# Kernel tuning notes

Measured on AMD Instinct MI355X. Metric: run time of the kernel, lower is better.

The kernel has to match this reference:

```python
import jax, jax.numpy as jnp
import numpy as np

H = 2048        # hidden_size
NH = 32         # num_heads
HD = H // NH    # head_dim = 64
S = 512         # seq_len
UP = 2          # upsample_ratio
SU = S * UP     # upsampled seq len = 1024
INTER = 5632    # GatedMLP intermediate: int(2048*4*2/3) rounded up to mult of 256
EPS = 1e-6
DEPTH = 1


def rmsnorm(x, w):
    var = jnp.mean(jnp.square(x), axis=-1, keepdims=True)
    return x * jax.lax.rsqrt(var + EPS) * w


def setup_inputs() -> dict:
    key = jax.random.key(0)
    ks = jax.random.split(key, 12)
    sc = 0.02
    return {
        "hidden_states": jax.random.normal(ks[0], (2, S, H), dtype=jnp.float32),
        "W_up": jax.random.normal(ks[1], (SU, S), dtype=jnp.float32) * sc,
        "b_up": jnp.zeros((SU,), dtype=jnp.float32),
        "attn_norm_w": jnp.ones((H,), dtype=jnp.float32),
        "Wq": jax.random.normal(ks[2], (H, H), dtype=jnp.float32) * sc,
        "Wk": jax.random.normal(ks[3], (H, H), dtype=jnp.float32) * sc,
        "Wv": jax.random.normal(ks[4], (H, H), dtype=jnp.float32) * sc,
        "Wo": jax.random.normal(ks[5], (H, H), dtype=jnp.float32) * sc,
        "mlp_norm_w": jnp.ones((H,), dtype=jnp.float32),
        "Wg": jax.random.normal(ks[6], (INTER, H), dtype=jnp.float32) * sc,
        "Wu": jax.random.normal(ks[7], (INTER, H), dtype=jnp.float32) * sc,
        "Wd": jax.random.normal(ks[8], (H, INTER), dtype=jnp.float32) * sc,
    }


def reference(hidden_states, W_up, b_up, attn_norm_w, Wq, Wk, Wv, Wo,
              mlp_norm_w, Wg, Wu, Wd):
    B = hidden_states.shape[0]
    # init_upsampled_tokens: Linear over the sequence axis
    # up[b,t,d] = sum_s h[b,s,d] * W_up[t,s] + b_up[t]
    up = jnp.einsum('bsd,ts->btd', hidden_states, W_up) + b_up[None, :, None]

    for _ in range(DEPTH):
        residual = jnp.concatenate([hidden_states, up], axis=-2)  # [B, S+SU, H]
        x = rmsnorm(up, attn_norm_w)                               # [B, SU, H]
        q = (x @ Wq.T).reshape(B, SU, NH, HD)
        k = (residual @ Wk.T).reshape(B, S + SU, NH, HD)
        v = (residual @ Wv.T).reshape(B, S + SU, NH, HD)
        # explicit (non-causal) cross-attention, full score matrix
        scores = jnp.einsum('bshd,bthd->bsht', q, k) / np.sqrt(HD).astype(np.float32)
        attn = jax.nn.softmax(scores, axis=-1)
        o = jnp.einsum('bsht,bthd->bshd', attn, v).reshape(B, SU, H)
        x = (o @ Wo.T) + x                 # residual onto the *normed* tokens
        x = rmsnorm(x, mlp_norm_w)
        mlp_out = (jax.nn.silu(x @ Wg.T) * (x @ Wu.T)) @ Wd.T
        up = mlp_out + x
    return up
```

## Files before the change

### kernel.cpp

```cpp
#include <hip/hip_runtime.h>

typedef __bf16 bf16;
typedef __bf16 bf16x8 __attribute__((ext_vector_type(8)));
typedef float  f32x4  __attribute__((ext_vector_type(4)));
typedef unsigned int u32x4 __attribute__((ext_vector_type(4)));

#define NB 2
#define SS 512
#define HH 2048
#define SUx 1024
#define TT 1536
#define INTERx 5632

__device__ __forceinline__ void gload16(const void* g, void* l)
{
    __builtin_amdgcn_global_load_lds(
        (const __attribute__((address_space(1))) void*)g,
        (__attribute__((address_space(3))) void*)l, 16, 0, 0);
}

struct CastArgs {
    const float* src[10];
    bf16*        dst[10];
    int          blk0[11];
};

__global__ __launch_bounds__(256)
void cast_all_k(CastArgs a)
{
    int b = blockIdx.x;
    int s = 0;
    #pragma unroll
    for (int i = 1; i < 10; ++i) if (b >= a.blk0[i]) s = i;
    long idx = ((long)(b - a.blk0[s]) * 256 + threadIdx.x) * 8;
    const float* in = a.src[s];
    bf16* out = a.dst[s];
    f32x4 va = *(const f32x4*)(in + idx);
    f32x4 vb = *(const f32x4*)(in + idx + 4);
    bf16x8 o;
    o[0]=(bf16)va[0]; o[1]=(bf16)va[1]; o[2]=(bf16)va[2]; o[3]=(bf16)va[3];
    o[4]=(bf16)vb[0]; o[5]=(bf16)vb[1]; o[6]=(bf16)vb[2]; o[7]=(bf16)vb[3];
    *(bf16x8*)(out + idx) = o;
}

template <typename TIN>
__global__ __launch_bounds__(256)
void transpose_k(const TIN* __restrict__ in, bf16* __restrict__ out,
                 int inRS, int outRS, int nz2,
                 long inZ1, long inZ2, long outZ1, long outZ2)
{
    __shared__ bf16 tile[64][65];
    int z1 = blockIdx.z / nz2, z2 = blockIdx.z % nz2;
    const TIN* ip = in + (long)z1*inZ1 + (long)z2*inZ2
                  + (long)blockIdx.x*64*inRS + (long)blockIdx.y*64;
    bf16* op = out + (long)z1*outZ1 + (long)z2*outZ2
             + (long)blockIdx.y*64*outRS + (long)blockIdx.x*64;
    int tc = threadIdx.x & 63, tr = threadIdx.x >> 6;
    #pragma unroll
    for (int rr = 0; rr < 64; rr += 4)
        tile[rr+tr][tc] = (bf16)(float)ip[(long)(rr+tr)*inRS + tc];
    __syncthreads();
    #pragma unroll
    for (int cc = 0; cc < 64; cc += 4)
        op[(long)(cc+tr)*outRS + tc] = tile[tc][cc+tr];
}

__global__ __launch_bounds__(256)
void rmsnorm_k(const float* __restrict__ x, const float* __restrict__ w,
               bf16* __restrict__ yb, float* __restrict__ yf)
{
    long row = blockIdx.x;
    const float* xp = x + row * HH;
    int t = threadIdx.x;
    f32x4 v0 = *(const f32x4*)(xp + t*8);
    f32x4 v1 = *(const f32x4*)(xp + t*8 + 4);
    float ss = 0.f;
    #pragma unroll
    for (int j = 0; j < 4; ++j) ss += v0[j]*v0[j] + v1[j]*v1[j];
    #pragma unroll
    for (int off = 32; off > 0; off >>= 1) ss += __shfl_xor(ss, off);
    __shared__ float red[4];
    if ((t & 63) == 0) red[t >> 6] = ss;
    __syncthreads();
    float tot = red[0] + red[1] + red[2] + red[3];
    float inv = rsqrtf(tot * (1.0f/(float)HH) + 1e-6f);
    f32x4 w0 = *(const f32x4*)(w + t*8);
    f32x4 w1 = *(const f32x4*)(w + t*8 + 4);
    f32x4 y0, y1; bf16x8 ob;
    #pragma unroll
    for (int j = 0; j < 4; ++j) {
        y0[j] = v0[j] * inv * w0[j];
        y1[j] = v1[j] * inv * w1[j];
        ob[j]   = (bf16)y0[j];
        ob[4+j] = (bf16)y1[j];
    }
    *(bf16x8*)(yb + row*HH + t*8) = ob;
    if (yf) {
        *(f32x4*)(yf + row*HH + t*8)     = y0;
        *(f32x4*)(yf + row*HH + t*8 + 4) = y1;
    }
}

template <int GU, int DEPTH>
__device__ __forceinline__
void gemm_body(const bf16* __restrict__ A, const bf16* __restrict__ Bw,
               int Nsplit, int K,
               long sA, long sB,
               bf16* __restrict__ Cb, bf16* __restrict__ Cb2, long sCb,
               float* __restrict__ C32, long sC32,
               const float* __restrict__ res, long sRes,
               const float* __restrict__ bias,
               float scale, int doSilu,
               int lin, int gx, int nwg,
               bf16* Asmem, bf16* Bsmem)
{
    int z = blockIdx.z;
    const bf16* Ap = A + (long)z * sA;

    int n0, m0;
    if (GU) {
        int c = lin & 7, off = lin >> 3;
        int gx8 = gx >> 3;
        int perStrip = gx8 * 8;
        int a = off / perStrip;
        int r = off - a * perStrip;
        int m = a * 8 + (r & 7);
        int nIdx = c * gx8 + (r >> 3);
        n0 = nIdx * 128; m0 = m * 128;
    } else {
        int qq = nwg >> 3, r8 = nwg & 7;
        int xcd = lin & 7, off = lin >> 3;
        int wg = (xcd < r8 ? xcd * (qq + 1) : r8 * (qq + 1) + (xcd - r8) * qq) + off;
        n0 = (wg % gx) * 128; m0 = (wg / gx) * 128;
    }

    int t = threadIdx.x, lane = t & 63, w = t >> 6;
    int wr = w >> 2, wc = w & 3;
    int lc = lane & 15, lg = lane >> 4;

    int lr = lane >> 3, ls = lane & 7;
    const bf16* gA[2]; const bf16* gB[2];
    int ldsOff[2];
    #pragma unroll
    for (int i = 0; i < 2; ++i) {
        int r = (i*8 + w)*8 + lr;
        gA[i] = Ap + (long)(m0 + r) * K + (ls ^ lr) * 8;
        if (GU) {
            long grow = (long)(n0 >> 1) + (r >> 1);
            gB[i] = Bw + ((r & 1) ? (long)INTERx * K : 0) + grow * K + (ls ^ lr) * 8;
        } else {
            const bf16* Bp = Bw + (long)z * sB;
            gB[i] = Bp + (long)(n0 + r) * K + (ls ^ lr) * 8;
        }
        ldsOff[i] = (i*8 + w) * 512;
    }

    f32x4 zero = {0.f, 0.f, 0.f, 0.f};
    f32x4 acc[4][2];
    #pragma unroll
    for (int i = 0; i < 4; ++i)
        #pragma unroll
        for (int j = 0; j < 2; ++j) acc[i][j] = zero;

    auto stage = [&](int buf, int ti) {
        long ko = (long)ti * 64;
        #pragma unroll
        for (int i = 0; i < 2; ++i) {
            gload16(gA[i] + ko, Asmem + buf*(128*64) + ldsOff[i]);
            gload16(gB[i] + ko, Bsmem + buf*(128*64) + ldsOff[i]);
        }
    };

    auto compute = [&](int buf) {
        const bf16* Asc = Asmem + buf * (128*64);
        const bf16* Bsc = Bsmem + buf * (128*64);
        #pragma unroll
        for (int kk = 0; kk < 2; ++kk) {
            bf16x8 af[4], bfv[2];
            #pragma unroll
            for (int i = 0; i < 4; ++i) {
                int rA = wr*64 + i*16 + lc;
                af[i]  = *(const bf16x8*)(Asc + rA*64 + (((kk*4 + lg) ^ (rA & 7)) * 8));
            }
            #pragma unroll
            for (int j = 0; j < 2; ++j) {
                int rB = wc*32 + j*16 + lc;
                bfv[j] = *(const bf16x8*)(Bsc + rB*64 + (((kk*4 + lg) ^ (rB & 7)) * 8));
            }
            __builtin_amdgcn_s_setprio(1);
            #pragma unroll
            for (int i = 0; i < 4; ++i)
                #pragma unroll
                for (int j = 0; j < 2; ++j)
                    acc[i][j] = __builtin_amdgcn_mfma_f32_16x16x32_bf16(af[i], bfv[j], acc[i][j], 0, 0, 0);
            __builtin_amdgcn_s_setprio(0);
        }
    };

    int NKI = K >> 6;
    if (DEPTH == 1) {
        for (int ks = 0; ks < NKI; ++ks) {
            stage(0, ks);
            asm volatile("s_waitcnt vmcnt(0)" ::: "memory");
            __builtin_amdgcn_s_barrier();
            __builtin_amdgcn_sched_barrier(0);
            compute(0);
            __builtin_amdgcn_s_barrier();
        }
    } else {
        #pragma unroll
        for (int d = 0; d < DEPTH; ++d)
            if (d < NKI) stage(d, d);
        int cur = 0;
        for (int ks = 0; ks < NKI; ++ks) {
            int ahead = NKI - 1 - ks;
            if (ahead > DEPTH - 1) ahead = DEPTH - 1;
            if      (DEPTH > 3 && ahead >= 3) asm volatile("s_waitcnt vmcnt(12)" ::: "memory");
            else if (DEPTH > 2 && ahead == 2) asm volatile("s_waitcnt vmcnt(8)"  ::: "memory");
            else if (ahead == 1)              asm volatile("s_waitcnt vmcnt(4)"  ::: "memory");
            else                              asm volatile("s_waitcnt vmcnt(0)"  ::: "memory");
            __builtin_amdgcn_s_barrier();
            __builtin_amdgcn_sched_barrier(0);
            compute(cur);
            __builtin_amdgcn_s_barrier();
            if (ks + DEPTH < NKI) stage(cur, ks + DEPTH);
            cur = (cur + 1 == DEPTH) ? 0 : cur + 1;
        }
    }

    if (GU) {
        #pragma unroll
        for (int i = 0; i < 4; ++i) {
            #pragma unroll
            for (int j = 0; j < 2; ++j) {
                int tc2 = wc*32 + j*16 + lc;
                int colp = (n0 >> 1) + (tc2 >> 1);
                #pragma unroll
                for (int r = 0; r < 4; ++r) {
                    int row = m0 + wr*64 + i*16 + lg*4 + r;
                    float v = acc[i][j][r];
                    float pv = __shfl_xor(v, 1);
                    float g  = (lc & 1) ? pv : v;
                    float uu = (lc & 1) ? v  : pv;
                    float prod = (g / (1.f + __expf(-g))) * uu;
                    if (!(lc & 1))
                        Cb[(long)row * Nsplit + colp] = (bf16)prod;
                }
            }
        }
    } else {
        #pragma unroll
        for (int i = 0; i < 4; ++i) {
            #pragma unroll
            for (int j = 0; j < 2; ++j) {
                int col = n0 + wc*32 + j*16 + lc;
                bf16* dst = Cb; int c2 = col;
                if (Cb2 && col >= Nsplit) { dst = Cb2; c2 = col - Nsplit; }
                int firstHalf = (col < Nsplit);
                #pragma unroll
                for (int r = 0; r < 4; ++r) {
                    int row = m0 + wr*64 + i*16 + lg*4 + r;
                    float v = acc[i][j][r] * scale;
                    if (bias)   v += bias[row];
                    if (doSilu && firstHalf) v = v / (1.f + __expf(-v));
                    long off = (long)row * Nsplit + c2;
                    if (res)  v += res[(long)z * sRes + off];
                    if (C32)  C32[(long)z * sC32 + off] = v;
                    if (dst)  dst[(long)z * sCb + off] = (bf16)v;
                }
            }
        }
    }
}

template <int GU, int DEPTH>
__global__ __launch_bounds__(512)
void gemm_k(const bf16* __restrict__ A, const bf16* __restrict__ Bw,
            int Nsplit, int K,
            long sA, long sB,
            bf16* __restrict__ Cb, bf16* __restrict__ Cb2, long sCb,
            float* __restrict__ C32, long sC32,
            const float* __restrict__ res, long sRes,
            const float* __restrict__ bias,
            float scale, int doSilu)
{
    __shared__ alignas(16) bf16 As[DEPTH][128 * 64];
    __shared__ alignas(16) bf16 Bs[DEPTH][128 * 64];
    int gx = gridDim.x;
    int nwg = gx * gridDim.y;
    int lin = blockIdx.y * gx + blockIdx.x;
    gemm_body<GU, DEPTH>(A, Bw, Nsplit, K, sA, sB, Cb, Cb2, sCb, C32, sC32,
                         res, sRes, bias, scale, doSilu, lin, gx, nwg,
                         &As[0][0], &Bs[0][0]);
}

__global__ __launch_bounds__(512)
void qkv_k(const bf16* __restrict__ x1b, const bf16* __restrict__ wq,
           bf16* __restrict__ qb,
           const bf16* __restrict__ resb, const bf16* __restrict__ wk,
           bf16* __restrict__ kb, bf16* __restrict__ vb)
{
    __shared__ alignas(16) bf16 As[128 * 64];
    __shared__ alignas(16) bf16 Bs[128 * 64];
    int lin = blockIdx.x;
    if (lin < 256) {
        gemm_body<0, 1>(x1b, wq, HH, HH, 0, 0, qb, nullptr, 0, nullptr, 0,
                        nullptr, 0, nullptr, 0.125f, 0, lin, 16, 256,
                        &As[0], &Bs[0]);
    } else {
        gemm_body<0, 1>(resb, wk, HH, HH, 0, 0, kb, vb, 0, nullptr, 0,
                        nullptr, 0, nullptr, 1.0f, 0, lin - 256, 32, 768,
                        &As[0], &Bs[0]);
    }
}

__global__ __launch_bounds__(512)
void attn_k(const bf16* __restrict__ q, const bf16* __restrict__ k,
            const bf16* __restrict__ vt, bf16* __restrict__ o)
{
    int qc = blockIdx.x, h = blockIdx.y, b = blockIdx.z;
    int t = threadIdx.x, lane = t & 63, w = t >> 6;
    int lc = lane & 15, lg = lane >> 4;
    const bf16* qp = q  + ((long)(b*SUx + qc*256 + w*32)) * HH + h*64;
    const bf16* kp = k  + ((long)b*TT) * HH + h*64;
    const bf16* vp = vt + ((long)(b*32 + h)) * 64 * TT;

    __shared__ alignas(16) bf16 Ks[2][64*64];
    __shared__ alignas(16) bf16 Vs[2][64*64];
    __shared__ alignas(16) bf16 Ps[8][2][16*72];

    bf16x8 qf[2][2];
    #pragma unroll
    for (int s = 0; s < 2; ++s)
        #pragma unroll
        for (int kk = 0; kk < 2; ++kk)
            qf[s][kk] = *(const bf16x8*)(qp + (long)(s*16 + lc)*HH + kk*32 + lg*8);

    int lr = lane >> 3, ls = lane & 7;
    int srow = w*8 + lr;
    int sslot = ls ^ lr;
    const bf16* gK = kp + (long)srow * HH + sslot*8;
    const bf16* gV = vp + (long)srow * TT + sslot*8;
    int ldsO = w * 512;

    f32x4 zero = {0.f, 0.f, 0.f, 0.f};
    f32x4 oacc[2][4];
    float lsum[2][4];
    #pragma unroll
    for (int qs = 0; qs < 2; ++qs) {
        #pragma unroll
        for (int r = 0; r < 4; ++r) lsum[qs][r] = 0.f;
        #pragma unroll
        for (int dt = 0; dt < 4; ++dt) oacc[qs][dt] = zero;
    }

    const int NS = TT / 64;
    gload16(gK,            &Ks[0][0] + ldsO);
    gload16(gV,            &Vs[0][0] + ldsO);
    gload16(gK + 64L*HH,   &Ks[1][0] + ldsO);
    gload16(gV + 64,       &Vs[1][0] + ldsO);

    for (int st = 0; st < NS; ++st) {
        int cur = st & 1;
        const bf16* Kc = &Ks[cur][0];
        const bf16* Vc = &Vs[cur][0];

        if (st == NS - 1) asm volatile("s_waitcnt vmcnt(0)" ::: "memory");
        else              asm volatile("s_waitcnt vmcnt(2)" ::: "memory");
        __builtin_amdgcn_s_barrier();
        __builtin_amdgcn_sched_barrier(0);

        bf16x8 kf[4][2];
        #pragma unroll
        for (int s2 = 0; s2 < 4; ++s2) {
            int row = s2*16 + lc;
            #pragma unroll
            for (int kk = 0; kk < 2; ++kk)
                kf[s2][kk] = *(const bf16x8*)(Kc + row*64 + (((kk*4 + lg) ^ (row & 7)) * 8));
        }
        f32x4 sv[2][4];
        __builtin_amdgcn_s_setprio(1);
        #pragma unroll
        for (int qs = 0; qs < 2; ++qs)
            #pragma unroll
            for (int s2 = 0; s2 < 4; ++s2) {
                f32x4 a0 = __builtin_amdgcn_mfma_f32_16x16x32_bf16(qf[qs][0], kf[s2][0], zero, 0, 0, 0);
                sv[qs][s2] = __builtin_amdgcn_mfma_f32_16x16x32_bf16(qf[qs][1], kf[s2][1], a0, 0, 0, 0);
            }
        __builtin_amdgcn_s_setprio(0);

        bf16* Pw = &Ps[w][0][0];
        #pragma unroll
        for (int qs = 0; qs < 2; ++qs)
            #pragma unroll
            for (int r = 0; r < 4; ++r) {
                int prow = lg*4 + r;
                #pragma unroll
                for (int s2 = 0; s2 < 4; ++s2) {
                    float pp = __expf(sv[qs][s2][r]);
                    lsum[qs][r] += pp;
                    Pw[qs*(16*72) + prow*72 + s2*16 + lc] = (bf16)pp;
                }
            }
        asm volatile("s_waitcnt lgkmcnt(0)" ::: "memory");
        __builtin_amdgcn_sched_barrier(0);

        bf16x8 pf[2][2];
        #pragma unroll
        for (int qs = 0; qs < 2; ++qs)
            #pragma unroll
            for (int ks = 0; ks < 2; ++ks)
                pf[qs][ks] = *(const bf16x8*)(Pw + qs*(16*72) + lc*72 + (ks*4 + lg)*8);
        bf16x8 vf[4][2];
        #pragma unroll
        for (int dt = 0; dt < 4; ++dt) {
            int row = dt*16 + lc;
            #pragma unroll
            for (int ks = 0; ks < 2; ++ks)
                vf[dt][ks] = *(const bf16x8*)(Vc + row*64 + (((ks*4 + lg) ^ (row & 7)) * 8));
        }
        __builtin_amdgcn_s_setprio(1);
        #pragma unroll
        for (int qs = 0; qs < 2; ++qs)
            #pragma unroll
            for (int dt = 0; dt < 4; ++dt) {
                oacc[qs][dt] = __builtin_amdgcn_mfma_f32_16x16x32_bf16(pf[qs][0], vf[dt][0], oacc[qs][dt], 0, 0, 0);
                oacc[qs][dt] = __builtin_amdgcn_mfma_f32_16x16x32_bf16(pf[qs][1], vf[dt][1], oacc[qs][dt], 0, 0, 0);
            }
        __builtin_amdgcn_s_setprio(0);

        __builtin_amdgcn_s_barrier();
        if (st + 2 < NS) {
            long t2 = (long)(st + 2) * 64;
            gload16(gK + t2*HH, (bf16*)Kc + ldsO);
            gload16(gV + t2,    (bf16*)Vc + ldsO);
        }
    }

    #pragma unroll
    for (int qs = 0; qs < 2; ++qs)
        #pragma unroll
        for (int r = 0; r < 4; ++r) {
            float l = lsum[qs][r];
            l += __shfl_xor(l, 1);
            l += __shfl_xor(l, 2);
            l += __shfl_xor(l, 4);
            l += __shfl_xor(l, 8);
            float inv = 1.0f / l;
            long row = (long)b*SUx + qc*256 + w*32 + qs*16 + lg*4 + r;
            #pragma unroll
            for (int dt = 0; dt < 4; ++dt)
                o[row*HH + h*64 + dt*16 + lc] = (bf16)(oacc[qs][dt][r] * inv);
        }
}

extern "C" void kernel_launch(void* const* d_in, const int* in_sizes, int n_in,
                              void* d_out, int out_size, void* d_ws, size_t ws_size,
                              hipStream_t stream)
{
    const float* hs  = (const float*)d_in[0];
    const float* Wup = (const float*)d_in[1];
    const float* bup = (const float*)d_in[2];
    const float* anw = (const float*)d_in[3];
    const float* Wq  = (const float*)d_in[4];
    const float* Wk  = (const float*)d_in[5];
    const float* Wv  = (const float*)d_in[6];
    const float* Wo  = (const float*)d_in[7];
    const float* mnw = (const float*)d_in[8];
    const float* Wg  = (const float*)d_in[9];
    const float* Wu  = (const float*)d_in[10];
    const float* Wd  = (const float*)d_in[11];
    float* outp = (float*)d_out;

    char* p = (char*)d_ws;
    auto take = [&](size_t bytes) -> void* {
        void* r = (void*)p;
        p += (bytes + 255) & ~(size_t)255;
        return r;
    };

    bf16* wq  = (bf16*)take((size_t)HH*HH*2);
    bf16* wk  = (bf16*)take(2 * (size_t)HH*HH*2);
    bf16* wv  = wk + (size_t)HH*HH;
    bf16* wo  = (bf16*)take((size_t)HH*HH*2);
    bf16* wgu = (bf16*)take(2 * (size_t)INTERx*HH*2);
    bf16* wd  = (bf16*)take((size_t)INTERx*HH*2);
    bf16* wup = (bf16*)take((size_t)SUx*SS*2);
    bf16* ht  = (bf16*)take((size_t)NB*HH*SS*2);
    bf16* resb= (bf16*)take((size_t)NB*TT*HH*2);
    float* x1f= (float*)take((size_t)NB*SUx*HH*4);
    bf16* x1b = (bf16*)take((size_t)NB*SUx*HH*2);
    float* upf= (float*)take((size_t)NB*SUx*HH*4);

    size_t attn_bytes = (size_t)NB*SUx*HH*2 + 3*(size_t)NB*TT*HH*2 + (size_t)NB*SUx*HH*2;
    size_t mlp_bytes  = (size_t)NB*SUx*HH*4 + (size_t)NB*SUx*HH*2 + (size_t)NB*SUx*INTERx*2;
    char* un = (char*)take(attn_bytes > mlp_bytes ? attn_bytes : mlp_bytes);
    bf16* qb  = (bf16*)un;
    bf16* kb  = qb  + (size_t)NB*SUx*HH;
    bf16* vb  = kb  + (size_t)NB*TT*HH;
    bf16* vtb = vb  + (size_t)NB*TT*HH;
    bf16* ob  = vtb + (size_t)NB*TT*HH;
    float* x2f= (float*)un;
    bf16* x2b = (bf16*)(un + (size_t)NB*SUx*HH*4);
    bf16* gb  = x2b + (size_t)NB*SUx*HH;

    CastArgs ca;
    int blk = 0;
    auto seg = [&](int i, const float* s, bf16* d, long nelem) {
        ca.src[i] = s; ca.dst[i] = d; ca.blk0[i] = blk;
        blk += (int)(nelem / 2048);
    };
    seg(0, Wq,  wq,  (long)HH*HH);
    seg(1, Wk,  wk,  (long)HH*HH);
    seg(2, Wv,  wv,  (long)HH*HH);
    seg(3, Wo,  wo,  (long)HH*HH);
    seg(4, Wg,  wgu, (long)INTERx*HH);
    seg(5, Wu,  wgu + (size_t)INTERx*HH, (long)INTERx*HH);
    seg(6, Wd,  wd,  (long)INTERx*HH);
    seg(7, Wup, wup, (long)SUx*SS);
    seg(8, hs,                 resb,                   (long)SS*HH);
    seg(9, hs + (size_t)SS*HH, resb + (size_t)TT*HH,   (long)SS*HH);
    ca.blk0[10] = blk;
    cast_all_k<<<dim3(blk), 256, 0, stream>>>(ca);

    transpose_k<float><<<dim3(SS/64, HH/64, NB), 256, 0, stream>>>(
        hs, ht, HH, SS, 1, (long)SS*HH, 0, (long)HH*SS, 0);

    gemm_k<0, 4><<<dim3(HH/128, SUx/128, NB), 512, 0, stream>>>(
        wup, ht, HH, SS, 0, (long)HH*SS,
        resb + (size_t)SS*HH, nullptr, (long)TT*HH,
        upf, (long)SUx*HH,
        nullptr, 0, bup, 1.0f, 0);

    rmsnorm_k<<<dim3(NB*SUx), 256, 0, stream>>>(upf, anw, x1b, x1f);

    qkv_k<<<dim3(1024), 512, 0, stream>>>(x1b, wq, qb, resb, wk, kb, vb);

    transpose_k<bf16><<<dim3(TT/64, 1, NB*32), 256, 0, stream>>>(
        vb, vtb, HH, TT, 32, (long)TT*HH, 64, (long)32*64*TT, (long)64*TT);

    attn_k<<<dim3(SUx/256, 32, NB), 512, 0, stream>>>(qb, kb, vtb, ob);

    gemm_k<0, 4><<<dim3(HH/128, (NB*SUx)/128, 1), 512, 0, stream>>>(
        ob, wo, HH, HH, 0, 0, nullptr, nullptr, 0, upf, 0, x1f, 0, nullptr, 1.0f, 0);

    rmsnorm_k<<<dim3(NB*SUx), 256, 0, stream>>>(upf, mnw, x2b, x2f);

    gemm_k<1, 1><<<dim3((2*INTERx)/128, (NB*SUx)/128, 1), 512, 0, stream>>>(
        x2b, wgu, INTERx, HH, 0, 0, gb, nullptr, 0, nullptr, 0, nullptr, 0, nullptr, 1.0f, 0);

    gemm_k<0, 4><<<dim3(HH/128, (NB*SUx)/128, 1), 512, 0, stream>>>(
        gb, wd, HH, INTERx, 0, 0, nullptr, nullptr, 0, outp, 0, x2f, 0, nullptr, 1.0f, 0);

    (void)in_sizes; (void)n_in; (void)out_size; (void)ws_size;
}
```

Measured before the change: 459.1 us.

## Add dedicated 256x128-tile gate/up GEMM kernel with fused interleaved SiLU epilogue

Replaces the generic gate/up GEMM launch with a specialized kernel that uses 256x128 output tiles and 8 waves each computing 64x64. B rows interleave gate and up weights so adjacent columns hold a gate/up pair, which are combined via lane shuffle into SiLU(g)*u. The larger M tile is meant to raise operand reuse per LDS load, and the kernel also uses a custom XCD-aware tile mapping with an occupancy hint. It drops the double-buffered pipelining and waits for all loads before each compute step, so load latency may be exposed.

```diff
diff --git a/kernel.cpp b/kernel.cpp
--- a/kernel.cpp
+++ b/kernel.cpp
@@ -118,16 +118,7 @@
     const bf16* Ap = A + (long)z * sA;
 
     int n0, m0;
-    if (GU) {
-        int c = lin & 7, off = lin >> 3;
-        int gx8 = gx >> 3;
-        int perStrip = gx8 * 8;
-        int a = off / perStrip;
-        int r = off - a * perStrip;
-        int m = a * 8 + (r & 7);
-        int nIdx = c * gx8 + (r >> 3);
-        n0 = nIdx * 128; m0 = m * 128;
-    } else {
+    {
         int qq = nwg >> 3, r8 = nwg & 7;
         int xcd = lin & 7, off = lin >> 3;
         int wg = (xcd < r8 ? xcd * (qq + 1) : r8 * (qq + 1) + (xcd - r8) * qq) + off;
@@ -292,6 +283,103 @@
     gemm_body<GU, DEPTH>(A, Bw, Nsplit, K, sA, sB, Cb, Cb2, sCb, C32, sC32,
                          res, sRes, bias, scale, doSilu, lin, gx, nwg,
                          &As[0][0], &Bs[0][0]);
+}
+
+__global__ __launch_bounds__(512, 4)
+void gemm_mlp_k(const bf16* __restrict__ A, const bf16* __restrict__ Bw,
+                int Nsplit, int K, bf16* __restrict__ Cb)
+{
+    __shared__ alignas(16) bf16 As[256 * 64];
+    __shared__ alignas(16) bf16 Bs[128 * 64];
+
+    int lin = blockIdx.x;
+    int c = lin & 7, off = lin >> 3;
+    int nIdx = c * 11 + off % 11;
+    int mIdx = off / 11;
+    int n0 = nIdx * 128, m0 = mIdx * 256;
+
+    int t = threadIdx.x, lane = t & 63, w = t >> 6;
+    int wrow = w >> 1, wcol = w & 1;
+    int lc = lane & 15, lg = lane >> 4;
+
+    int sr = t >> 3, ss_ = t & 7;
+    const bf16* gA[4]; const bf16* gB[2];
+    int ldsA[4], ldsB[2];
+    #pragma unroll
+    for (int i = 0; i < 4; ++i) {
+        int r = i*64 + sr;
+        gA[i] = A + (long)(m0 + r) * K + ((ss_ ^ (r & 7)) * 8);
+        ldsA[i] = i * 4096 + t * 8;
+    }
+    #pragma unroll
+    for (int i = 0; i < 2; ++i) {
+        int r = i*64 + sr;
+        long grow = (long)(n0 >> 1) + (r >> 1);
+        gB[i] = Bw + ((r & 1) ? (long)INTERx * K : 0) + grow * K + ((ss_ ^ (r & 7)) * 8);
+        ldsB[i] = i * 4096 + t * 8;
+    }
+
+    f32x4 zero = {0.f, 0.f, 0.f, 0.f};
+    f32x4 acc[4][4];
+    #pragma unroll
+    for (int i = 0; i < 4; ++i)
+        #pragma unroll
+        for (int j = 0; j < 4; ++j) acc[i][j] = zero;
+
+    int NKI = K >> 6;
+    for (int ks = 0; ks < NKI; ++ks) {
+        long ko = (long)ks * 64;
+        #pragma unroll
+        for (int i = 0; i < 4; ++i) gload16(gA[i] + ko, As + ldsA[i]);
+        #pragma unroll
+        for (int i = 0; i < 2; ++i) gload16(gB[i] + ko, Bs + ldsB[i]);
+        asm volatile("s_waitcnt vmcnt(0)" ::: "memory");
+        __builtin_amdgcn_s_barrier();
+        __builtin_amdgcn_sched_barrier(0);
+
+        #pragma unroll
+        for (int kk = 0; kk < 2; ++kk) {
+            bf16x8 af[4], bfv[4];
+            #pragma unroll
+            for (int i = 0; i < 4; ++i) {
+                int rA = wrow*64 + i*16 + lc;
+                af[i]  = *(const bf16x8*)(As + rA*64 + (((kk*4 + lg) ^ (rA & 7)) * 8));
+            }
+            #pragma unroll
+            for (int j = 0; j < 4; ++j) {
+                int rB = wcol*64 + j*16 + lc;
+                bfv[j] = *(const bf16x8*)(Bs + rB*64 + (((kk*4 + lg) ^ (rB & 7)) * 8));
+            }
+            __builtin_amdgcn_s_setprio(1);
+            #pragma unroll
+            for (int i = 0; i < 4; ++i)
+                #pragma unroll
+                for (int j = 0; j < 4; ++j)
+                    acc[i][j] = __builtin_amdgcn_mfma_f32_16x16x32_bf16(af[i], bfv[j], acc[i][j], 0, 0, 0);
+            __builtin_amdgcn_s_setprio(0);
+        }
+        __builtin_amdgcn_s_barrier();
+    }
+
+    #pragma unroll
+    for (int i = 0; i < 4; ++i) {
+        #pragma unroll
+        for (int j = 0; j < 4; ++j) {
+            int tc2 = wcol*64 + j*16 + lc;
+            int colp = (n0 >> 1) + (tc2 >> 1);
+            #pragma unroll
+            for (int r = 0; r < 4; ++r) {
+                int row = m0 + wrow*64 + i*16 + lg*4 + r;
+                float v = acc[i][j][r];
+                float pv = __shfl_xor(v, 1);
+                float g  = (lc & 1) ? pv : v;
+                float uu = (lc & 1) ? v  : pv;
+                float prod = (g / (1.f + __expf(-g))) * uu;
+                if (!(lc & 1))
+                    Cb[(long)row * Nsplit + colp] = (bf16)prod;
+            }
+        }
+    }
 }
 
 __global__ __launch_bounds__(512)
@@ -546,8 +634,7 @@
 
     rmsnorm_k<<<dim3(NB*SUx), 256, 0, stream>>>(upf, mnw, x2b, x2f);
 
-    gemm_k<1, 1><<<dim3((2*INTERx)/128, (NB*SUx)/128, 1), 512, 0, stream>>>(
-        x2b, wgu, INTERx, HH, 0, 0, gb, nullptr, 0, nullptr, 0, nullptr, 0, nullptr, 1.0f, 0);
+    gemm_mlp_k<<<dim3(704), 512, 0, stream>>>(x2b, wgu, INTERx, HH, gb);
 
     gemm_k<0, 4><<<dim3(HH/128, (NB*SUx)/128, 1), 512, 0, stream>>>(
         gb, wd, HH, INTERx, 0, 0, nullptr, nullptr, 0, outp, 0, x2f, 0, nullptr, 1.0f, 0);
```

Result: no change. 465.9 us (+1.5%).

## Split-K the down projection into two partials and reduce with residual

Applied to the files above, without the earlier changes.

The down-projection GEMM (K=5632) now runs as two K-halves over the grid z-dimension, writing fp32 partial outputs to two new workspace buffers. A separate reduce kernel then sums the partials and adds the residual. A leading-dimension parameter is added to the GEMM so that K-slices can stride over the full row. The aim is to double the number of workgroups for a 256-tile GEMM and so fill the GPU better. The cost is extra fp32 traffic and one more launch. The gate/up GEMM also drops its custom strip-based tile mapping in favour of the generic XCD-aware remap, and the down GEMM's pipeline depth goes from 4 to 2.

```diff
diff --git a/kernel.cpp b/kernel.cpp
--- a/kernel.cpp
+++ b/kernel.cpp
@@ -43,6 +43,23 @@
     *(bf16x8*)(out + idx) = o;
 }
 
+__global__ __launch_bounds__(256)
+void reduce2_k(const float* __restrict__ p0, const float* __restrict__ p1,
+               const float* __restrict__ res, float* __restrict__ out)
+{
+    long i = ((long)blockIdx.x * 256 + threadIdx.x) * 8;
+    #pragma unroll
+    for (int h = 0; h < 2; ++h) {
+        f32x4 a = *(const f32x4*)(p0 + i + h*4);
+        f32x4 b = *(const f32x4*)(p1 + i + h*4);
+        f32x4 c = *(const f32x4*)(res + i + h*4);
+        f32x4 o;
+        #pragma unroll
+        for (int j = 0; j < 4; ++j) o[j] = a[j] + b[j] + c[j];
+        *(f32x4*)(out + i + h*4) = o;
+    }
+}
+
 template <typename TIN>
 __global__ __launch_bounds__(256)
 void transpose_k(const TIN* __restrict__ in, bf16* __restrict__ out,
@@ -104,7 +121,7 @@
 template <int GU, int DEPTH>
 __device__ __forceinline__
 void gemm_body(const bf16* __restrict__ A, const bf16* __restrict__ Bw,
-               int Nsplit, int K,
+               int Nsplit, int K, int ldk,
                long sA, long sB,
                bf16* __restrict__ Cb, bf16* __restrict__ Cb2, long sCb,
                float* __restrict__ C32, long sC32,
@@ -118,16 +135,7 @@
     const bf16* Ap = A + (long)z * sA;
 
     int n0, m0;
-    if (GU) {
-        int c = lin & 7, off = lin >> 3;
-        int gx8 = gx >> 3;
-        int perStrip = gx8 * 8;
-        int a = off / perStrip;
-        int r = off - a * perStrip;
-        int m = a * 8 + (r & 7);
-        int nIdx = c * gx8 + (r >> 3);
-        n0 = nIdx * 128; m0 = m * 128;
-    } else {
+    {
         int qq = nwg >> 3, r8 = nwg & 7;
         int xcd = lin & 7, off = lin >> 3;
         int wg = (xcd < r8 ? xcd * (qq + 1) : r8 * (qq + 1) + (xcd - r8) * qq) + off;
@@ -144,13 +152,13 @@
     #pragma unroll
     for (int i = 0; i < 2; ++i) {
         int r = (i*8 + w)*8 + lr;
-        gA[i] = Ap + (long)(m0 + r) * K + (ls ^ lr) * 8;
+        gA[i] = Ap + (long)(m0 + r) * ldk + (ls ^ lr) * 8;
         if (GU) {
             long grow = (long)(n0 >> 1) + (r >> 1);
-            gB[i] = Bw + ((r & 1) ? (long)INTERx * K : 0) + grow * K + (ls ^ lr) * 8;
+            gB[i] = Bw + ((r & 1) ? (long)INTERx * ldk : 0) + grow * ldk + (ls ^ lr) * 8;
         } else {
             const bf16* Bp = Bw + (long)z * sB;
-            gB[i] = Bp + (long)(n0 + r) * K + (ls ^ lr) * 8;
+            gB[i] = Bp + (long)(n0 + r) * ldk + (ls ^ lr) * 8;
         }
         ldsOff[i] = (i*8 + w) * 512;
     }
@@ -276,7 +284,7 @@
 template <int GU, int DEPTH>
 __global__ __launch_bounds__(512)
 void gemm_k(const bf16* __restrict__ A, const bf16* __restrict__ Bw,
-            int Nsplit, int K,
+            int Nsplit, int K, int ldk,
             long sA, long sB,
             bf16* __restrict__ Cb, bf16* __restrict__ Cb2, long sCb,
             float* __restrict__ C32, long sC32,
@@ -289,7 +297,7 @@
     int gx = gridDim.x;
     int nwg = gx * gridDim.y;
     int lin = blockIdx.y * gx + blockIdx.x;
-    gemm_body<GU, DEPTH>(A, Bw, Nsplit, K, sA, sB, Cb, Cb2, sCb, C32, sC32,
+    gemm_body<GU, DEPTH>(A, Bw, Nsplit, K, ldk, sA, sB, Cb, Cb2, sCb, C32, sC32,
                          res, sRes, bias, scale, doSilu, lin, gx, nwg,
                          &As[0][0], &Bs[0][0]);
 }
@@ -304,11 +312,11 @@
     __shared__ alignas(16) bf16 Bs[128 * 64];
     int lin = blockIdx.x;
     if (lin < 256) {
-        gemm_body<0, 1>(x1b, wq, HH, HH, 0, 0, qb, nullptr, 0, nullptr, 0,
+        gemm_body<0, 1>(x1b, wq, HH, HH, HH, 0, 0, qb, nullptr, 0, nullptr, 0,
                         nullptr, 0, nullptr, 0.125f, 0, lin, 16, 256,
                         &As[0], &Bs[0]);
     } else {
-        gemm_body<0, 1>(resb, wk, HH, HH, 0, 0, kb, vb, 0, nullptr, 0,
+        gemm_body<0, 1>(resb, wk, HH, HH, HH, 0, 0, kb, vb, 0, nullptr, 0,
                         nullptr, 0, nullptr, 1.0f, 0, lin - 256, 32, 768,
                         &As[0], &Bs[0]);
     }
@@ -491,6 +499,8 @@
     float* x1f= (float*)take((size_t)NB*SUx*HH*4);
     bf16* x1b = (bf16*)take((size_t)NB*SUx*HH*2);
     float* upf= (float*)take((size_t)NB*SUx*HH*4);
+    float* pk0= (float*)take((size_t)NB*SUx*HH*4);
+    float* pk1= (float*)take((size_t)NB*SUx*HH*4);
 
     size_t attn_bytes = (size_t)NB*SUx*HH*2 + 3*(size_t)NB*TT*HH*2 + (size_t)NB*SUx*HH*2;
     size_t mlp_bytes  = (size_t)NB*SUx*HH*4 + (size_t)NB*SUx*HH*2 + (size_t)NB*SUx*INTERx*2;
@@ -527,7 +537,7 @@
         hs, ht, HH, SS, 1, (long)SS*HH, 0, (long)HH*SS, 0);
 
     gemm_k<0, 4><<<dim3(HH/128, SUx/128, NB), 512, 0, stream>>>(
-        wup, ht, HH, SS, 0, (long)HH*SS,
+        wup, ht, HH, SS, SS, 0, (long)HH*SS,
         resb + (size_t)SS*HH, nullptr, (long)TT*HH,
         upf, (long)SUx*HH,
         nullptr, 0, bup, 1.0f, 0);
@@ -542,15 +552,23 @@
     attn_k<<<dim3(SUx/256, 32, NB), 512, 0, stream>>>(qb, kb, vtb, ob);
 
     gemm_k<0, 4><<<dim3(HH/128, (NB*SUx)/128, 1), 512, 0, stream>>>(
-        ob, wo, HH, HH, 0, 0, nullptr, nullptr, 0, upf, 0, x1f, 0, nullptr, 1.0f, 0);
+        ob, wo, HH, HH, HH, 0, 0, nullptr, nullptr, 0, upf, 0, x1f, 0, nullptr, 1.0f, 0);
 
     rmsnorm_k<<<dim3(NB*SUx), 256, 0, stream>>>(upf, mnw, x2b, x2f);
 
     gemm_k<1, 1><<<dim3((2*INTERx)/128, (NB*SUx)/128, 1), 512, 0, stream>>>(
-        x2b, wgu, INTERx, HH, 0, 0, gb, nullptr, 0, nullptr, 0, nullptr, 0, nullptr, 1.0f, 0);
-
-    gemm_k<0, 4><<<dim3(HH/128, (NB*SUx)/128, 1), 512, 0, stream>>>(
-        gb, wd, HH, INTERx, 0, 0, nullptr, nullptr, 0, outp, 0, x2f, 0, nullptr, 1.0f, 0);
+        x2b, wgu, INTERx, HH, HH, 0, 0, gb, nullptr, 0, nullptr, 0, nullptr, 0, nullptr, 1.0f, 0);
+
+    gemm_k<0, 2><<<dim3(HH/128, (NB*SUx)/128, 2), 512, 0, stream>>>(
+        gb, wd, HH, INTERx/2, INTERx,
+        (long)(INTERx/2),
+        (long)(INTERx/2),
+        nullptr, nullptr, 0,
+        pk0, (long)(pk1 - pk0),
+        nullptr, 0, nullptr, 1.0f, 0);
+
+    reduce2_k<<<dim3((unsigned)((size_t)NB*SUx*HH/2048)), 256, 0, stream>>>(
+        pk0, pk1, x2f, outp);
 
     (void)in_sizes; (void)n_in; (void)out_size; (void)ws_size;
 }
```

Result: no change. 462.5 us (+0.7%).
